# Performance work log

Measured on AMD Instinct MI355X. Metric: run time of the kernel, lower is better.

## Reference

```python
import jax, jax.numpy as jnp
import numpy as np

B, T, E, V = 128, 64, 300, 50000
C, HI, WI = 512, 14, 14
HID, K, L = 1024, 512, 2


def setup_inputs() -> dict:
    key = jax.random.key(0)
    ks = jax.random.split(key, 16)
    s = 0.05
    return {
        "desc": jax.random.randint(ks[0], (B, T), 0, V),
        "img": jax.random.normal(ks[1], (B, C, HI, WI), jnp.float32),
        "emb": jax.random.normal(ks[2], (V, E), jnp.float32) * 0.1,
        "W_ih": jax.random.normal(ks[3], (4 * HID, E), jnp.float32) * s,
        "W_hh": jax.random.normal(ks[4], (4 * HID, HID), jnp.float32) * s,
        "b_ih": jnp.zeros((4 * HID,), jnp.float32),
        "b_hh": jnp.zeros((4 * HID,), jnp.float32),
        "W_img": jax.random.normal(ks[5], (HID, C), jnp.float32) * s,
        "b_img": jnp.zeros((HID,), jnp.float32),
        "Wl_img": jax.random.normal(ks[6], (L, K, HID), jnp.float32) * s,
        "Wl_q": jax.random.normal(ks[7], (L, K, HID), jnp.float32) * s,
        "bl_q": jnp.zeros((L, K), jnp.float32),
        "wl_p": jax.random.normal(ks[8], (L, K), jnp.float32) * s,
        "bl_p": jnp.zeros((L,), jnp.float32),
    }


def _lstm_last(x, W_ih, W_hh, b_ih, b_hh):
    # x: [T, B, E]; returns last-step hidden state h_T: [B, HID]
    hid = W_hh.shape[1]
    h0 = jnp.zeros((x.shape[1], hid), x.dtype)

    def step(carry, xt):
        h, c = carry
        g = xt @ W_ih.T + b_ih + h @ W_hh.T + b_hh
        i, f, gg, o = jnp.split(g, 4, axis=-1)  # torch gate order i,f,g,o
        c = jax.nn.sigmoid(f) * c + jax.nn.sigmoid(i) * jnp.tanh(gg)
        h = jax.nn.sigmoid(o) * jnp.tanh(c)
        return (h, c), None

    (h, _), _ = jax.lax.scan(step, (h0, h0), x)
    return h


def reference(desc, img, emb, W_ih, W_hh, b_ih, b_hh, W_img, b_img,
              Wl_img, Wl_q, bl_q, wl_p, bl_p):
    # --- text branch ---
    e = emb[desc]                       # [B, T, E] embedding gather
    x = e.reshape(T, B, E)              # faithful: torch uses reshape, NOT transpose
    u_k = _lstm_last(x, W_ih, W_hh, b_ih, b_hh)  # [B, HID]

    # --- image branch ---
    n_areas = HI * WI
    img_r = img.reshape(B, n_areas, C)  # faithful: reshape, NOT permute
    out_img = img_r @ W_img.T + b_img   # [B, N, HID]

    # --- stacked additive attention ---
    for i in range(L):
        t_img = out_img @ Wl_img[i].T                      # [B, N, K]
        t_u = u_k @ Wl_q[i].T + bl_q[i]                    # [B, K]
        h_a = jnp.tanh(t_img + t_u[:, None, :])            # [B, N, K]
        p = jax.nn.softmax(h_a @ wl_p[i] + bl_p[i], axis=1)  # [B, N]
        temp = out_img.reshape(B, HID, n_areas)            # faithful reshape
        v = jnp.einsum("bhn,bn->bh", temp, p)              # [B, HID]
        u_k = v + u_k
    return u_k
```

## Files before the change

kernel.cpp:

```cpp
#include <hip/hip_runtime.h>
#include <hip/hip_bf16.h>

#define B_    128
#define T_    64
#define E_    300
#define HID_  1024
#define G4_   4096
#define C_    512
#define NA_   196
#define KATT_ 512
#define MIMG_ 25088

typedef short s16x8 __attribute__((ext_vector_type(8)));
typedef float f32x4 __attribute__((ext_vector_type(4)));

__device__ __forceinline__ unsigned short f2bf(float f) {
  __hip_bfloat16 h = __float2bfloat16(f);
  return __builtin_bit_cast(unsigned short, h);
}
__device__ __forceinline__ float bf2f(unsigned short u) {
  __hip_bfloat16 h = __builtin_bit_cast(__hip_bfloat16, u);
  return __bfloat162float(h);
}

__global__ __launch_bounds__(256) void conv_bf16(const float* __restrict__ in,
                                                 unsigned short* __restrict__ out,
                                                 int n) {
  int i = blockIdx.x * 256 + threadIdx.x;
  if (i < n) out[i] = f2bf(in[i]);
}

__global__ __launch_bounds__(256) void conv_pad320(const float* __restrict__ in,
                                                   unsigned short* __restrict__ out,
                                                   int rows) {
  int i = blockIdx.x * 256 + threadIdx.x;
  if (i >= rows * 320) return;
  int r = i / 320, k = i - r * 320;
  out[i] = (k < 300) ? f2bf(in[(size_t)r * 300 + k]) : (unsigned short)0;
}

__global__ __launch_bounds__(256) void gather_emb(const int* __restrict__ desc,
                                                  const float* __restrict__ emb,
                                                  unsigned short* __restrict__ out) {
  int i = blockIdx.x * 256 + threadIdx.x;
  int m = i / 320, k = i - m * 320;
  float v = (k < 300) ? emb[(size_t)desc[m] * 300 + k] : 0.f;
  out[i] = f2bf(v);
}

__global__ __launch_bounds__(256) void gemm_mfma(
    const unsigned short* __restrict__ A, int lda,
    const unsigned short* __restrict__ Bw, int Kd,
    const float* __restrict__ bias, const float* __restrict__ bias2,
    float* __restrict__ Cf, unsigned short* __restrict__ Cb, int ldc,
    int mode, const float* __restrict__ tu, const float* __restrict__ wp,
    float* __restrict__ sc)
{
  __shared__ unsigned short As[128 * 40];
  __shared__ unsigned short Bs[128 * 40];
  const int tid = threadIdx.x;
  const int m0 = blockIdx.y << 7, n0 = blockIdx.x << 7;
  const int w = tid >> 6, l = tid & 63;
  const int wr = w >> 1, wc = w & 1;
  const int lrow = l & 15, lk = (l >> 4) << 3;
  const int srow = tid >> 2, schunk = (tid & 3) << 3;

  f32x4 acc[4][4];
#pragma unroll
  for (int i = 0; i < 4; i++)
#pragma unroll
    for (int j = 0; j < 4; j++) acc[i][j] = (f32x4){0.f, 0.f, 0.f, 0.f};

  const unsigned short* Ap = A + (size_t)(m0 + srow) * lda + schunk;
  const unsigned short* Bp = Bw + (size_t)(n0 + srow) * Kd + schunk;
  const size_t arep = (size_t)64 * lda, brep = (size_t)64 * Kd;

  for (int k0 = 0; k0 < Kd; k0 += 32) {
    *(uint4*)&As[srow * 40 + schunk]        = *(const uint4*)(Ap + k0);
    *(uint4*)&As[(srow + 64) * 40 + schunk] = *(const uint4*)(Ap + arep + k0);
    *(uint4*)&Bs[srow * 40 + schunk]        = *(const uint4*)(Bp + k0);
    *(uint4*)&Bs[(srow + 64) * 40 + schunk] = *(const uint4*)(Bp + brep + k0);
    __syncthreads();
    s16x8 af[4], bfr[4];
#pragma unroll
    for (int i = 0; i < 4; i++) {
      af[i]  = *(const s16x8*)&As[(wr * 64 + i * 16 + lrow) * 40 + lk];
      bfr[i] = *(const s16x8*)&Bs[(wc * 64 + i * 16 + lrow) * 40 + lk];
    }
#pragma unroll
    for (int i = 0; i < 4; i++)
#pragma unroll
      for (int j = 0; j < 4; j++)
        acc[i][j] = __builtin_amdgcn_mfma_f32_16x16x32_bf16(af[i], bfr[j], acc[i][j], 0, 0, 0);
    __syncthreads();
  }

  const int quad = l >> 4;
  if (mode == 3) {
#pragma unroll
    for (int i = 0; i < 4; i++) {
#pragma unroll
      for (int r = 0; r < 4; r++) {
        int row = m0 + wr * 64 + i * 16 + quad * 4 + r;
        int b = row / NA_;
        float partial = 0.f;
#pragma unroll
        for (int j = 0; j < 4; j++) {
          int col = n0 + wc * 64 + j * 16 + lrow;
          float v = acc[i][j][r] + tu[(size_t)b * KATT_ + col];
          partial += tanhf(v) * wp[col];
        }
        partial += __shfl_xor(partial, 1);
        partial += __shfl_xor(partial, 2);
        partial += __shfl_xor(partial, 4);
        partial += __shfl_xor(partial, 8);
        if (lrow == 0) unsafeAtomicAdd(&sc[row], partial);
      }
    }
    return;
  }

#pragma unroll
  for (int i = 0; i < 4; i++) {
    int rbase = m0 + wr * 64 + i * 16 + quad * 4;
#pragma unroll
    for (int j = 0; j < 4; j++) {
      int col = n0 + wc * 64 + j * 16 + lrow;
      float badd = (bias ? bias[col] : 0.f) + (bias2 ? bias2[col] : 0.f);
#pragma unroll
      for (int r = 0; r < 4; r++) {
        float v = acc[i][j][r] + badd;
        int m = rbase + r;
        if (mode == 0)      Cf[(size_t)m * ldc + col] = v;
        else if (mode == 1) Cb[(size_t)m * ldc + col] = f2bf(v);
        else {
          size_t off = ((size_t)(m >> 7)) * 524288 + (size_t)col * 128 + (m & 127);
          Cb[off] = f2bf(v);
        }
      }
    }
  }
}

__global__ __launch_bounds__(512) void lstm_step2(
    const unsigned short* __restrict__ hin,
    const unsigned short* __restrict__ Xg_t,
    const unsigned short* __restrict__ Whh,
    float* __restrict__ cbuf,
    unsigned short* __restrict__ hout,
    float* __restrict__ u,
    unsigned short* __restrict__ ub)
{
  __shared__ unsigned short Bs[32 * 1024];
  const int tid = threadIdx.x;
  const int w = tid >> 6, l = tid & 63;
  const int mb = blockIdx.x & 1, jb = blockIdx.x >> 1;
  const int mt = w & 3, nt = w >> 2;
  const int quad = l >> 4, nl = l & 15;
  const int g = l & 3, jjl = (l >> 2) & 3;

  const int brow_a = mb * 64 + mt * 16 + nl;
  const int bq = mb * 64 + mt * 16 + quad * 4;
  const int j = jb * 8 + nt * 4 + jjl;
  const int col = (g << 10) + j;
  const int nrow = nt * 16 + nl;

  ushort4 xg4 = *(const ushort4*)(Xg_t + (size_t)col * 128 + bq);
  float4 c4 = *(const float4*)(cbuf + (size_t)j * 128 + bq);

  for (int i = tid; i < 4096; i += 512) {
    int r = i >> 7, ch = i & 127;
    int wrow = (r & 3) * 1024 + jb * 8 + (r >> 2);
    uint4 v = *(const uint4*)(Whh + (size_t)wrow * 1024 + ch * 8);
    *(uint4*)&Bs[r * 1024 + (ch ^ (r & 7)) * 8] = v;
  }
  __syncthreads();

  const unsigned short* Ap = hin + (size_t)brow_a * 1024;
  f32x4 acc0 = {0.f,0.f,0.f,0.f}, acc1 = {0.f,0.f,0.f,0.f};
#pragma unroll
  for (int kc = 0; kc < 32; kc++) {
    s16x8 a = *(const s16x8*)(Ap + (kc << 5) + (quad << 3));
    int slot = ((kc << 2) | quad) ^ (nrow & 7);
    s16x8 b = *(const s16x8*)&Bs[nrow * 1024 + (slot << 3)];
    if (kc & 1) acc1 = __builtin_amdgcn_mfma_f32_16x16x32_bf16(a, b, acc1, 0, 0, 0);
    else        acc0 = __builtin_amdgcn_mfma_f32_16x16x32_bf16(a, b, acc0, 0, 0, 0);
  }
  f32x4 acc = acc0 + acc1;

  float cn4[4], hn4[4];
#pragma unroll
  for (int r = 0; r < 4; r++) {
    unsigned short xr = (r == 0) ? xg4.x : (r == 1) ? xg4.y : (r == 2) ? xg4.z : xg4.w;
    float v = acc[r] + bf2f(xr);
    float x1 = __shfl_xor(v, 1);
    float x2 = __shfl_xor(v, 2);
    float x3 = __shfl_xor(x1, 2);
    float gi = (g == 0) ? v  : (g == 1) ? x1 : (g == 2) ? x2 : x3;
    float gf = (g == 0) ? x1 : (g == 1) ? v  : (g == 2) ? x3 : x2;
    float gg = (g == 0) ? x2 : (g == 1) ? x3 : (g == 2) ? v  : x1;
    float go = (g == 0) ? x3 : (g == 1) ? x2 : (g == 2) ? x1 : v;
    float si = 1.f / (1.f + expf(-gi));
    float sf = 1.f / (1.f + expf(-gf));
    float so = 1.f / (1.f + expf(-go));
    float cprev = (r == 0) ? c4.x : (r == 1) ? c4.y : (r == 2) ? c4.z : c4.w;
    float cn = sf * cprev + si * tanhf(gg);
    cn4[r] = cn;
    hn4[r] = so * tanhf(cn);
  }
  if (g == 0) {
    float4 co = {cn4[0], cn4[1], cn4[2], cn4[3]};
    *(float4*)(cbuf + (size_t)j * 128 + bq) = co;
#pragma unroll
    for (int r = 0; r < 4; r++)
      hout[(size_t)(bq + r) * 1024 + j] = f2bf(hn4[r]);
    if (u) {
#pragma unroll
      for (int r = 0; r < 4; r++) {
        size_t idx = (size_t)(bq + r) * 1024 + j;
        u[idx] = hn4[r];
        ub[idx] = f2bf(hn4[r]);
      }
    }
  }
}

__global__ __launch_bounds__(512) void tu_gemm(
    const unsigned short* __restrict__ ub, const unsigned short* __restrict__ Wq,
    const float* __restrict__ bq, float* __restrict__ tu)
{
  __shared__ unsigned short Bs[16 * 1032];
  const int tid = threadIdx.x;
  const int w = tid >> 6, l = tid & 63;
  const int n0 = blockIdx.x << 4;
  const int quad = l >> 4, nl = l & 15;
  for (int i = tid; i < 2048; i += 512) {
    int r = i >> 7, ch = i & 127;
    *(uint4*)&Bs[r * 1032 + ch * 8] = *(const uint4*)(Wq + (size_t)(n0 + r) * 1024 + ch * 8);
  }
  __syncthreads();
  const unsigned short* Ap = ub + (size_t)(w * 16 + nl) * 1024;
  f32x4 acc0 = {0.f,0.f,0.f,0.f}, acc1 = {0.f,0.f,0.f,0.f};
#pragma unroll 8
  for (int kc = 0; kc < 32; kc++) {
    s16x8 a = *(const s16x8*)(Ap + (kc << 5) + (quad << 3));
    s16x8 b = *(const s16x8*)&Bs[nl * 1032 + (kc << 5) + (quad << 3)];
    if (kc & 1) acc1 = __builtin_amdgcn_mfma_f32_16x16x32_bf16(a, b, acc1, 0, 0, 0);
    else        acc0 = __builtin_amdgcn_mfma_f32_16x16x32_bf16(a, b, acc0, 0, 0, 0);
  }
  f32x4 acc = acc0 + acc1;
  int colg = n0 + nl;
  float badd = bq[colg];
#pragma unroll
  for (int r = 0; r < 4; r++)
    tu[(size_t)(w * 16 + quad * 4 + r) * KATT_ + colg] = acc[r] + badd;
}

__global__ __launch_bounds__(256) void softmax_pool2(
    const float* __restrict__ sc, const unsigned short* __restrict__ outimg,
    float* __restrict__ u)
{
  int hg = blockIdx.x, b = blockIdx.y, tid = threadIdx.x;
  __shared__ float p[NA_];
  __shared__ float red[8];
  float v = (tid < NA_) ? sc[b * NA_ + tid] : -1e30f;
  float m = v;
#pragma unroll
  for (int off = 32; off; off >>= 1) m = fmaxf(m, __shfl_down(m, off, 64));
  if ((tid & 63) == 0) red[tid >> 6] = m;
  __syncthreads();
  float bm = fmaxf(fmaxf(red[0], red[1]), fmaxf(red[2], red[3]));
  float e = (tid < NA_) ? expf(v - bm) : 0.f;
  float s = e;
#pragma unroll
  for (int off = 32; off; off >>= 1) s += __shfl_down(s, off, 64);
  if ((tid & 63) == 0) red[4 + (tid >> 6)] = s;
  __syncthreads();
  float bs = red[4] + red[5] + red[6] + red[7];
  if (tid < NA_) p[tid] = e / bs;
  __syncthreads();
  int h = hg * 128 + (tid >> 1);
  int half = tid & 1;
  const unsigned short* r = outimg + (size_t)b * (HID_ * NA_) + (size_t)h * NA_ + half * 98;
  float acc = 0.f;
#pragma unroll 7
  for (int n = 0; n < 98; n += 2) {
    unsigned int pk = *(const unsigned int*)(r + n);
    acc += bf2f((unsigned short)(pk & 0xffff)) * p[half * 98 + n];
    acc += bf2f((unsigned short)(pk >> 16))    * p[half * 98 + n + 1];
  }
  acc += __shfl_xor(acc, 1);
  if (half == 0) u[(size_t)b * HID_ + h] += acc;
}

extern "C" void kernel_launch(void* const* d_in, const int* in_sizes, int n_in,
                              void* d_out, int out_size, void* d_ws, size_t ws_size,
                              hipStream_t stream) {
  const int*   desc   = (const int*)  d_in[0];
  const float* img    = (const float*)d_in[1];
  const float* emb    = (const float*)d_in[2];
  const float* W_ih   = (const float*)d_in[3];
  const float* W_hh   = (const float*)d_in[4];
  const float* b_ih   = (const float*)d_in[5];
  const float* b_hh   = (const float*)d_in[6];
  const float* W_img  = (const float*)d_in[7];
  const float* b_img  = (const float*)d_in[8];
  const float* Wl_img = (const float*)d_in[9];
  const float* Wl_q   = (const float*)d_in[10];
  const float* bl_q   = (const float*)d_in[11];
  const float* wl_p   = (const float*)d_in[12];
  float* u = (float*)d_out;

  uint8_t* base = (uint8_t*)d_ws;
  unsigned short* Xgb    = (unsigned short*)(base);
  unsigned short* imgb   = (unsigned short*)(base);
  unsigned short* outimg = (unsigned short*)(base + 67108864);
  unsigned short* Whhb   = (unsigned short*)(base + 118489088);
  unsigned short* Wihb   = (unsigned short*)(base + 126877696);
  unsigned short* Aemb   = (unsigned short*)(base + 129499136);
  unsigned short* Wimgb  = (unsigned short*)(base + 134742016);
  unsigned short* Wlimgb = (unsigned short*)(base + 135790592);
  unsigned short* Wlqb   = (unsigned short*)(base + 137887744);
  unsigned short* ubb    = (unsigned short*)(base + 139984896);
  unsigned short* h0b    = (unsigned short*)(base + 140247040);
  unsigned short* h1b    = (unsigned short*)(base + 140509184);
  float*          tub    = (float*)(base + 140771328);
  float*          scb0   = (float*)(base + 141033472);
  float*          scb1   = (float*)(base + 141133824);
  float*          cbuf   = (float*)(base + 141234176);

  conv_bf16<<<(G4_ * HID_ + 255) / 256, 256, 0, stream>>>(W_hh, Whhb, G4_ * HID_);
  conv_pad320<<<(G4_ * 320 + 255) / 256, 256, 0, stream>>>(W_ih, Wihb, G4_);
  gather_emb<<<(8192 * 320) / 256, 256, 0, stream>>>(desc, emb, Aemb);
  conv_bf16<<<(HID_ * C_ + 255) / 256, 256, 0, stream>>>(W_img, Wimgb, HID_ * C_);
  conv_bf16<<<(2 * KATT_ * HID_ + 255) / 256, 256, 0, stream>>>(Wl_img, Wlimgb, 2 * KATT_ * HID_);
  conv_bf16<<<(2 * KATT_ * HID_ + 255) / 256, 256, 0, stream>>>(Wl_q, Wlqb, 2 * KATT_ * HID_);

  hipMemsetAsync(h0b, 0, 262144, stream);
  hipMemsetAsync(cbuf, 0, 524288, stream);
  hipMemsetAsync(scb0, 0, 200704, stream);

  gemm_mfma<<<dim3(32, 64), 256, 0, stream>>>(Aemb, 320, Wihb, 320, b_ih, b_hh,
                                              nullptr, Xgb, 0, 2, nullptr, nullptr, nullptr);

  for (int t = 0; t < T_; t++) {
    const unsigned short* hi = (t & 1) ? h1b : h0b;
    unsigned short* ho = (t & 1) ? h0b : h1b;
    lstm_step2<<<256, 512, 0, stream>>>(hi, Xgb + (size_t)t * 524288, Whhb, cbuf, ho,
                                        (t == T_ - 1) ? u : nullptr,
                                        (t == T_ - 1) ? ubb : nullptr);
  }

  conv_bf16<<<(MIMG_ * C_ + 255) / 256, 256, 0, stream>>>(img, imgb, MIMG_ * C_);
  gemm_mfma<<<dim3(8, 196), 256, 0, stream>>>(imgb, C_, Wimgb, C_, b_img, nullptr,
                                              nullptr, outimg, HID_, 1, nullptr, nullptr, nullptr);

  for (int i = 0; i < 2; i++) {
    float* scb = (i == 0) ? scb0 : scb1;
    if (i == 1)
      conv_bf16<<<512, 256, 0, stream>>>(u, ubb, B_ * HID_);
    tu_gemm<<<32, 512, 0, stream>>>(ubb, Wlqb + (size_t)i * KATT_ * HID_,
                                    bl_q + i * KATT_, tub);
    gemm_mfma<<<dim3(4, 196), 256, 0, stream>>>(outimg, HID_,
                                                Wlimgb + (size_t)i * KATT_ * HID_, HID_,
                                                nullptr, nullptr, nullptr, nullptr, 0, 3,
                                                tub, wl_p + i * KATT_, scb);
    softmax_pool2<<<dim3(8, B_), 256, 0, stream>>>(scb, outimg, u);
  }
}
```

Baseline: 1.349 ms.

## Prepack W_hh into MFMA fragment order and drop LDS staging in LSTM step

W_hh is converted once into a layout where each lane's MFMA B-fragment is contiguous, so the LSTM step kernel reads its B operands straight from global memory (L2) with coalesced 16-byte loads instead of staging a 64KB tile into LDS and synchronising each step. This removes the per-step LDS fill and barrier across the 64 sequential launches. The input-projection GEMM epilogue also writes packed ushort4 stores in the transposed mode instead of scalar stores. The cost is that every wave now fetches B directly from global memory, which relies on L2 hits.

```diff
diff --git a/kernel.cpp b/kernel.cpp
--- a/kernel.cpp
+++ b/kernel.cpp
@@ -46,6 +46,17 @@
   int m = i / 320, k = i - m * 320;
   float v = (k < 300) ? emb[(size_t)desc[m] * 300 + k] : 0.f;
   out[i] = f2bf(v);
+}
+
+__global__ __launch_bounds__(256) void conv_whh(const float* __restrict__ in,
+                                                unsigned short* __restrict__ out) {
+  int o = blockIdx.x * 256 + threadIdx.x;
+  int e = o & 7, lq = (o >> 3) & 63, kc = (o >> 9) & 31, seg = o >> 14;
+  int nl = lq & 15, quad = lq >> 4;
+  int jb = seg >> 1, nt = seg & 1;
+  int r = nt * 16 + nl;
+  int wrow = (r & 3) * 1024 + jb * 8 + (r >> 2);
+  out[o] = f2bf(in[(size_t)wrow * 1024 + kc * 32 + quad * 8 + e]);
 }
 
 __global__ __launch_bounds__(256) void gemm_mfma(
@@ -127,31 +138,36 @@
     for (int j = 0; j < 4; j++) {
       int col = n0 + wc * 64 + j * 16 + lrow;
       float badd = (bias ? bias[col] : 0.f) + (bias2 ? bias2[col] : 0.f);
-#pragma unroll
-      for (int r = 0; r < 4; r++) {
-        float v = acc[i][j][r] + badd;
-        int m = rbase + r;
-        if (mode == 0)      Cf[(size_t)m * ldc + col] = v;
-        else if (mode == 1) Cb[(size_t)m * ldc + col] = f2bf(v);
-        else {
-          size_t off = ((size_t)(m >> 7)) * 524288 + (size_t)col * 128 + (m & 127);
-          Cb[off] = f2bf(v);
+      if (mode == 2) {
+        ushort4 pk;
+        pk.x = f2bf(acc[i][j][0] + badd);
+        pk.y = f2bf(acc[i][j][1] + badd);
+        pk.z = f2bf(acc[i][j][2] + badd);
+        pk.w = f2bf(acc[i][j][3] + badd);
+        size_t off = ((size_t)(rbase >> 7)) * 524288 + (size_t)col * 128 + (rbase & 127);
+        *(ushort4*)&Cb[off] = pk;
+      } else {
+#pragma unroll
+        for (int r = 0; r < 4; r++) {
+          float v = acc[i][j][r] + badd;
+          int m = rbase + r;
+          if (mode == 0) Cf[(size_t)m * ldc + col] = v;
+          else           Cb[(size_t)m * ldc + col] = f2bf(v);
         }
       }
     }
   }
 }
 
-__global__ __launch_bounds__(512) void lstm_step2(
+__global__ __launch_bounds__(512) void lstm_step3(
     const unsigned short* __restrict__ hin,
     const unsigned short* __restrict__ Xg_t,
-    const unsigned short* __restrict__ Whh,
+    const unsigned short* __restrict__ Whp,
     float* __restrict__ cbuf,
     unsigned short* __restrict__ hout,
     float* __restrict__ u,
     unsigned short* __restrict__ ub)
 {
-  __shared__ unsigned short Bs[32 * 1024];
   const int tid = threadIdx.x;
   const int w = tid >> 6, l = tid & 63;
   const int mb = blockIdx.x & 1, jb = blockIdx.x >> 1;
@@ -163,26 +179,18 @@
   const int bq = mb * 64 + mt * 16 + quad * 4;
   const int j = jb * 8 + nt * 4 + jjl;
   const int col = (g << 10) + j;
-  const int nrow = nt * 16 + nl;
 
   ushort4 xg4 = *(const ushort4*)(Xg_t + (size_t)col * 128 + bq);
   float4 c4 = *(const float4*)(cbuf + (size_t)j * 128 + bq);
 
-  for (int i = tid; i < 4096; i += 512) {
-    int r = i >> 7, ch = i & 127;
-    int wrow = (r & 3) * 1024 + jb * 8 + (r >> 2);
-    uint4 v = *(const uint4*)(Whh + (size_t)wrow * 1024 + ch * 8);
-    *(uint4*)&Bs[r * 1024 + (ch ^ (r & 7)) * 8] = v;
-  }
-  __syncthreads();
-
-  const unsigned short* Ap = hin + (size_t)brow_a * 1024;
+  const unsigned short* Ap = hin + (size_t)brow_a * 1024 + (quad << 3);
+  const unsigned short* Bp = Whp + (((size_t)(jb * 2 + nt)) << 14) + (l << 3);
+
   f32x4 acc0 = {0.f,0.f,0.f,0.f}, acc1 = {0.f,0.f,0.f,0.f};
 #pragma unroll
   for (int kc = 0; kc < 32; kc++) {
-    s16x8 a = *(const s16x8*)(Ap + (kc << 5) + (quad << 3));
-    int slot = ((kc << 2) | quad) ^ (nrow & 7);
-    s16x8 b = *(const s16x8*)&Bs[nrow * 1024 + (slot << 3)];
+    s16x8 a = *(const s16x8*)(Ap + (kc << 5));
+    s16x8 b = *(const s16x8*)(Bp + (kc << 9));
     if (kc & 1) acc1 = __builtin_amdgcn_mfma_f32_16x16x32_bf16(a, b, acc1, 0, 0, 0);
     else        acc0 = __builtin_amdgcn_mfma_f32_16x16x32_bf16(a, b, acc0, 0, 0, 0);
   }
@@ -315,7 +323,7 @@
   unsigned short* Xgb    = (unsigned short*)(base);
   unsigned short* imgb   = (unsigned short*)(base);
   unsigned short* outimg = (unsigned short*)(base + 67108864);
-  unsigned short* Whhb   = (unsigned short*)(base + 118489088);
+  unsigned short* Whp    = (unsigned short*)(base + 118489088);
   unsigned short* Wihb   = (unsigned short*)(base + 126877696);
   unsigned short* Aemb   = (unsigned short*)(base + 129499136);
   unsigned short* Wimgb  = (unsigned short*)(base + 134742016);
@@ -329,7 +337,7 @@
   float*          scb1   = (float*)(base + 141133824);
   float*          cbuf   = (float*)(base + 141234176);
 
-  conv_bf16<<<(G4_ * HID_ + 255) / 256, 256, 0, stream>>>(W_hh, Whhb, G4_ * HID_);
+  conv_whh<<<16384, 256, 0, stream>>>(W_hh, Whp);
   conv_pad320<<<(G4_ * 320 + 255) / 256, 256, 0, stream>>>(W_ih, Wihb, G4_);
   gather_emb<<<(8192 * 320) / 256, 256, 0, stream>>>(desc, emb, Aemb);
   conv_bf16<<<(HID_ * C_ + 255) / 256, 256, 0, stream>>>(W_img, Wimgb, HID_ * C_);
@@ -346,7 +354,7 @@
   for (int t = 0; t < T_; t++) {
     const unsigned short* hi = (t & 1) ? h1b : h0b;
     unsigned short* ho = (t & 1) ? h0b : h1b;
-    lstm_step2<<<256, 512, 0, stream>>>(hi, Xgb + (size_t)t * 524288, Whhb, cbuf, ho,
+    lstm_step3<<<256, 512, 0, stream>>>(hi, Xgb + (size_t)t * 524288, Whp, cbuf, ho,
                                         (t == T_ - 1) ? u : nullptr,
                                         (t == T_ - 1) ? ubb : nullptr);
   }
```

New measurement: 1.377 ms. 1.02x slower.
